# Optimization experiments

Hardware: AMD Instinct MI355X
Metric: run time of the kernel (lower is better)

Reference implementation:

```python
import jax, jax.numpy as jnp
import numpy as np

B, S, D = 8, 1024, 1024
H = 16
HD = D // H
FFN = 4096
BN = 64  # adapter bottleneck
ADAPTER_SCALE = 0.1
EPS = 1e-5


def _ln(x, g, b):
    m = jnp.mean(x, axis=-1, keepdims=True)
    v = jnp.mean(jnp.square(x - m), axis=-1, keepdims=True)
    return (x - m) * jax.lax.rsqrt(v + EPS) * g + b


def setup_inputs() -> dict:
    key = jax.random.key(0)
    ks = jax.random.split(key, 16)
    sd = 0.02
    # weights stored [in, out] (math identical to torch's x @ W.T with W [out,in])
    return {
        "x": jax.random.normal(ks[0], (B, S, D), jnp.float32),
        "ln1_g": jnp.ones((D,), jnp.float32),
        "ln1_b": jnp.zeros((D,), jnp.float32),
        "wq": jax.random.normal(ks[1], (D, D), jnp.float32) * sd,
        "wk": jax.random.normal(ks[2], (D, D), jnp.float32) * sd,
        "wv": jax.random.normal(ks[3], (D, D), jnp.float32) * sd,
        "wo": jax.random.normal(ks[4], (D, D), jnp.float32) * sd,
        "bo": jnp.zeros((D,), jnp.float32),
        "ln2_g": jnp.ones((D,), jnp.float32),
        "ln2_b": jnp.zeros((D,), jnp.float32),
        "w1": jax.random.normal(ks[5], (D, FFN), jnp.float32) * sd,
        "b1": jnp.zeros((FFN,), jnp.float32),
        "w2": jax.random.normal(ks[6], (FFN, D), jnp.float32) * sd,
        "b2": jnp.zeros((D,), jnp.float32),
        "aln_g": jnp.ones((D,), jnp.float32),
        "aln_b": jnp.zeros((D,), jnp.float32),
        "wd": jax.random.normal(ks[7], (D, BN), jnp.float32) * sd,
        "bd": jnp.zeros((BN,), jnp.float32),
        "wu": jax.random.normal(ks[8], (BN, D), jnp.float32) * sd,
        "bu": jnp.zeros((D,), jnp.float32),
    }


def reference(x, ln1_g, ln1_b, wq, wk, wv, wo, bo, ln2_g, ln2_b,
              w1, b1, w2, b2, aln_g, aln_b, wd, bd, wu, bu):
    b, s, d = x.shape
    scale = HD ** -0.5

    # --- attention branch ---
    h = _ln(x, ln1_g, ln1_b)
    q = (h @ wq).reshape(b, s, H, HD)
    k = (h @ wk).reshape(b, s, H, HD)
    v = (h @ wv).reshape(b, s, H, HD)
    scores = jnp.einsum('bqhd,bkhd->bhqk', q, k) * scale  # [B,H,S,S]
    probs = jax.nn.softmax(scores, axis=-1)
    attn = jnp.einsum('bhqk,bkhd->bqhd', probs, v).reshape(b, s, d)
    x = x + (attn @ wo + bo)

    # --- parallel adapter (LN-in, down-relu-up, scaled, no residual) ---
    a = _ln(x, aln_g, aln_b)
    adapt_x = (jax.nn.relu(a @ wd + bd) @ wu + bu) * ADAPTER_SCALE

    # --- MLP branch ---
    residual = x
    h2 = _ln(x, ln2_g, ln2_b)
    h2 = jax.nn.gelu(h2 @ w1 + b1, approximate=False)
    h2 = h2 @ w2 + b2
    h2 = h2 + adapt_x
    return residual + h2
```

## Files before the change

### kernel.cpp

```cpp
#include <hip/hip_runtime.h>
#include <hip/hip_bf16.h>
#include <cstdint>
#include <cstddef>

#define DI __device__ __forceinline__

typedef __attribute__((ext_vector_type(8))) short v8s;
typedef __attribute__((ext_vector_type(4))) float v4f;

DI void gload_lds16(const unsigned short* g, unsigned short* l) {
  __builtin_amdgcn_global_load_lds(
      (const __attribute__((address_space(1))) unsigned int*)g,
      (__attribute__((address_space(3))) unsigned int*)l, 16, 0, 0);
}

DI float bf2f(unsigned short u) { return __uint_as_float(((unsigned int)u) << 16); }
DI unsigned short f2bf(float f) {
  unsigned int u = __float_as_uint(f);
  u += 0x7FFFu + ((u >> 16) & 1u);
  return (unsigned short)(u >> 16);
}
DI unsigned int pack2(float a, float b) {
  return (unsigned int)f2bf(a) | ((unsigned int)f2bf(b) << 16);
}

__global__ __launch_bounds__(256) void transpose_cvt_k(
    const float* __restrict__ in, unsigned short* __restrict__ out, int R, int C) {
  __shared__ unsigned short t[32][33];
  const int j0 = blockIdx.x * 32, i0 = blockIdx.y * 32;
  const int tx = threadIdx.x & 31, ty = threadIdx.x >> 5;
#pragma unroll
  for (int r = 0; r < 32; r += 8) t[ty + r][tx] = f2bf(in[(size_t)(i0 + ty + r) * C + j0 + tx]);
  __syncthreads();
#pragma unroll
  for (int r = 0; r < 32; r += 8) out[(size_t)(j0 + ty + r) * R + i0 + tx] = t[tx][ty + r];
}

__global__ __launch_bounds__(256) void vtrans_k(
    const unsigned short* __restrict__ v, unsigned short* __restrict__ vt, int ld) {
  __shared__ unsigned short t[32][33];
  const int bh = blockIdx.z, b = bh >> 4, h = bh & 15;
  const int s0 = blockIdx.x * 32, d0 = blockIdx.y * 32;
  const int tx = threadIdx.x & 31, ty = threadIdx.x >> 5;
  const unsigned short* src = v + (size_t)(b * 1024 + s0) * ld + h * 64 + d0;
#pragma unroll
  for (int r = 0; r < 32; r += 8) t[ty + r][tx] = src[(size_t)(ty + r) * ld + tx];
  __syncthreads();
  unsigned short* dst = vt + ((size_t)bh * 64 + d0) * 1024 + s0;
#pragma unroll
  for (int r = 0; r < 32; r += 8) dst[(size_t)(ty + r) * 1024 + tx] = t[tx][ty + r];
}

__global__ __launch_bounds__(256) void ln_k(
    const float* __restrict__ x, const float* __restrict__ g,
    const float* __restrict__ b, unsigned short* __restrict__ out) {
  const int row = blockIdx.x;
  const float4 v = ((const float4*)(x + (size_t)row * 1024))[threadIdx.x];
  float s = v.x + v.y + v.z + v.w;
  float ss = v.x * v.x + v.y * v.y + v.z * v.z + v.w * v.w;
#pragma unroll
  for (int o = 1; o < 64; o <<= 1) { s += __shfl_xor(s, o); ss += __shfl_xor(ss, o); }
  __shared__ float red[8];
  const int wid = threadIdx.x >> 6, lane = threadIdx.x & 63;
  if (!lane) { red[wid] = s; red[4 + wid] = ss; }
  __syncthreads();
  s = red[0] + red[1] + red[2] + red[3];
  ss = red[4] + red[5] + red[6] + red[7];
  const float mean = s * (1.f / 1024.f);
  const float var = ss * (1.f / 1024.f) - mean * mean;
  const float rs = rsqrtf(var + 1e-5f);
  const float4 gv = ((const float4*)g)[threadIdx.x];
  const float4 bv = ((const float4*)b)[threadIdx.x];
  ushort4 ov;
  ov.x = f2bf((v.x - mean) * rs * gv.x + bv.x);
  ov.y = f2bf((v.y - mean) * rs * gv.y + bv.y);
  ov.z = f2bf((v.z - mean) * rs * gv.z + bv.z);
  ov.w = f2bf((v.w - mean) * rs * gv.w + bv.w);
  ((ushort4*)(out + (size_t)row * 1024))[threadIdx.x] = ov;
}

enum { EPI_NONE = 0, EPI_BIAS_RES = 1, EPI_GELU = 2, EPI_RELU = 3, EPI_SCALE_BIAS = 4, EPI_FINAL = 5 };

template <int BM, int BN, int EPI, typename CT>
__global__ __launch_bounds__(512, 2) void gemm8_k(
    const unsigned short* __restrict__ A, const unsigned short* __restrict__ Bt,
    CT* __restrict__ C, const float* __restrict__ bias,
    const float* __restrict__ res, const float* __restrict__ extra,
    int M, int N, int K, int gm, int gn) {
  constexpr int MF = BM / 32, NF = BN / 64, MPP = MF / 4;
  constexpr int LA = BM / 64, LB = BN / 64, LT = LA + LB;
  constexpr int BUFE = (BM + BN) * 64;
  __shared__ unsigned short lds[BUFE * 2];
  const int tid = threadIdx.x;
  const int lane = tid & 63, wid = tid >> 6;
  const int wm = wid >> 2, wn = wid & 3;
  const int l15 = lane & 15, l4 = lane >> 4;
  const int nwg = gm * gn;
  const int bid = blockIdx.x;
  const int swz = (bid % 8) * (nwg / 8) + bid / 8;
  const int row0 = (swz / gn) * BM, col0 = (swz % gn) * BN;
  const int NT = K >> 6;

  const int srow = tid >> 3, sgr = tid & 7;
  auto stA = [&](int kt, int b, int a) {
    const unsigned short* s = A + (size_t)(row0 + a * 64 + srow) * K + kt * 64 + ((sgr ^ (srow & 7)) << 3);
    gload_lds16(s, lds + b * BUFE + a * 4096 + tid * 8);
  };
  auto stB = [&](int kt, int b, int a) {
    const unsigned short* s = Bt + (size_t)(col0 + a * 64 + srow) * K + kt * 64 + ((sgr ^ (srow & 7)) << 3);
    gload_lds16(s, lds + b * BUFE + BM * 64 + a * 4096 + tid * 8);
  };

#pragma unroll
  for (int e = 0; e < LA; ++e) stA(0, 0, e);
#pragma unroll
  for (int e = 0; e < LB; ++e) stB(0, 0, e);
#pragma unroll
  for (int e = 0; e < LB; ++e) stB(1, 1, e);
  asm volatile("s_waitcnt vmcnt(%0)" ::"n"(LB) : "memory");
  __builtin_amdgcn_s_barrier();

  v4f acc[MF][NF] = {};
  v8s bfr[NF][2];
  for (int t = 0; t < NT; ++t) {
    const int buf = t & 1;
    const unsigned short* La = lds + buf * BUFE;
    const unsigned short* Lb = lds + buf * BUFE + BM * 64;
#pragma unroll
    for (int p = 0; p < 4; ++p) {
      if (p == 0) {
#pragma unroll
        for (int nf = 0; nf < NF; ++nf) {
          const int r = wn * (BN / 4) + nf * 16 + l15;
#pragma unroll
          for (int kk = 0; kk < 2; ++kk)
            bfr[nf][kk] = *(const v8s*)(Lb + r * 64 + ((kk * 32 + l4 * 8) ^ ((r & 7) << 3)));
        }
      }
      v8s af[MPP][2];
#pragma unroll
      for (int mm = 0; mm < MPP; ++mm) {
        const int r = wm * (BM / 2) + (p * MPP + mm) * 16 + l15;
#pragma unroll
        for (int kk = 0; kk < 2; ++kk)
          af[mm][kk] = *(const v8s*)(La + r * 64 + ((kk * 32 + l4 * 8) ^ ((r & 7) << 3)));
      }
#pragma unroll
      for (int e = p * LT / 4; e < (p + 1) * LT / 4; ++e) {
        if (e < LA) { if (t + 1 < NT) stA(t + 1, buf ^ 1, e); }
        else        { if (t + 2 < NT) stB(t + 2, buf, e - LA); }
      }
      __builtin_amdgcn_s_barrier();
      asm volatile("s_waitcnt lgkmcnt(0)" ::: "memory");
      __builtin_amdgcn_s_setprio(1);
#pragma unroll
      for (int mm = 0; mm < MPP; ++mm)
#pragma unroll
        for (int nf = 0; nf < NF; ++nf)
#pragma unroll
          for (int kk = 0; kk < 2; ++kk)
            acc[p * MPP + mm][nf] = __builtin_amdgcn_mfma_f32_16x16x32_bf16(
                af[mm][kk], bfr[nf][kk], acc[p * MPP + mm][nf], 0, 0, 0);
      __builtin_amdgcn_s_setprio(0);
      if (p == 3 && t + 1 < NT) {
        if (t + 2 < NT) asm volatile("s_waitcnt vmcnt(%0)" ::"n"(LB) : "memory");
        else            asm volatile("s_waitcnt vmcnt(0)" ::: "memory");
      }
      __builtin_amdgcn_s_barrier();
    }
  }

#pragma unroll
  for (int mf = 0; mf < MF; ++mf) {
#pragma unroll
    for (int nf = 0; nf < NF; ++nf) {
      const int col = col0 + wn * (BN / 4) + nf * 16 + l15;
      float bv = 0.f;
      if (EPI != EPI_NONE) bv = bias[col];
#pragma unroll
      for (int j = 0; j < 4; ++j) {
        const int row = row0 + wm * (BM / 2) + mf * 16 + l4 * 4 + j;
        const size_t idx = (size_t)row * N + col;
        float v = acc[mf][nf][j];
        if (EPI == EPI_BIAS_RES) v += bv + res[idx];
        else if (EPI == EPI_GELU) { v += bv; v = 0.5f * v * (1.f + erff(v * 0.70710678118f)); }
        else if (EPI == EPI_RELU) { v += bv; v = fmaxf(v, 0.f); }
        else if (EPI == EPI_SCALE_BIAS) { v = (v + bv) * 0.1f; }
        else if (EPI == EPI_FINAL) { v += bv + res[idx] + extra[idx]; }
        if constexpr (sizeof(CT) == 2) C[idx] = f2bf(v); else C[idx] = v;
      }
    }
  }
}

template <int BN, int EPI, typename CT>
__global__ __launch_bounds__(256) void gemm_k(
    const unsigned short* __restrict__ A, const unsigned short* __restrict__ Bt,
    CT* __restrict__ C, const float* __restrict__ bias,
    const float* __restrict__ res, const float* __restrict__ extra,
    int M, int N, int K) {
  constexpr int BM = 128, BK = 32;
  constexpr int WN = (BN == 128) ? 2 : 1;
  constexpr int MR = (BN == 128) ? 4 : 2;
  constexpr int NR = 4;
  __shared__ unsigned short sA[BM * BK];
  __shared__ unsigned short sB[BN * BK];
  const int tid = threadIdx.x;
  const int lane = tid & 63, wid = tid >> 6;
  const int wm = wid / WN, wn = wid % WN;
  const int l15 = lane & 15, l4 = lane >> 4;
  const int row0 = blockIdx.x * BM, col0 = blockIdx.y * BN;
  v4f acc[MR][NR] = {};
  const int rowA = wm * MR * 16;
  const int rowB = wn * NR * 16;
  for (int k0 = 0; k0 < K; k0 += BK) {
#pragma unroll
    for (int r = 0; r < (BM * BK) / (256 * 8); ++r) {
      int e = (r * 256 + tid) * 8;
      gload_lds16(A + (size_t)(row0 + (e >> 5)) * K + k0 + (e & 31), ((unsigned short*)sA) + e);
    }
#pragma unroll
    for (int r = 0; r < (BN * BK) / (256 * 8); ++r) {
      int e = (r * 256 + tid) * 8;
      gload_lds16(Bt + (size_t)(col0 + (e >> 5)) * K + k0 + (e & 31), ((unsigned short*)sB) + e);
    }
    __syncthreads();
    v8s af[MR], bfr2[NR];
#pragma unroll
    for (int m = 0; m < MR; ++m) af[m] = *(const v8s*)(sA + (rowA + m * 16 + l15) * BK + l4 * 8);
#pragma unroll
    for (int n = 0; n < NR; ++n) bfr2[n] = *(const v8s*)(sB + (rowB + n * 16 + l15) * BK + l4 * 8);
#pragma unroll
    for (int m = 0; m < MR; ++m)
#pragma unroll
      for (int n = 0; n < NR; ++n)
        acc[m][n] = __builtin_amdgcn_mfma_f32_16x16x32_bf16(af[m], bfr2[n], acc[m][n], 0, 0, 0);
    __syncthreads();
  }
#pragma unroll
  for (int m = 0; m < MR; ++m) {
#pragma unroll
    for (int n = 0; n < NR; ++n) {
      const int col = col0 + rowB + n * 16 + l15;
      float bv = 0.f;
      if (EPI != EPI_NONE) bv = bias[col];
#pragma unroll
      for (int j = 0; j < 4; ++j) {
        const int row = row0 + rowA + m * 16 + l4 * 4 + j;
        const size_t idx = (size_t)row * N + col;
        float v = acc[m][n][j];
        if (EPI == EPI_BIAS_RES) v += bv + res[idx];
        else if (EPI == EPI_GELU) { v += bv; v = 0.5f * v * (1.f + erff(v * 0.70710678118f)); }
        else if (EPI == EPI_RELU) { v += bv; v = fmaxf(v, 0.f); }
        else if (EPI == EPI_SCALE_BIAS) { v = (v + bv) * 0.1f; }
        else if (EPI == EPI_FINAL) { v += bv + res[idx] + extra[idx]; }
        if constexpr (sizeof(CT) == 2) C[idx] = f2bf(v); else C[idx] = v;
      }
    }
  }
}

__global__ __launch_bounds__(256) void attn_k(
    const unsigned short* __restrict__ Q, const unsigned short* __restrict__ Kc,
    const unsigned short* __restrict__ VT, unsigned short* __restrict__ O, int ldqk) {
  const int bh = blockIdx.y, b = bh >> 4, h = bh & 15;
  const int q0 = blockIdx.x * 64;
  const int tid = threadIdx.x, lane = tid & 63, wid = tid >> 6;
  const int l15 = lane & 15, l4 = lane >> 4;
  __shared__ unsigned short sQ[64 * 64];
  __shared__ unsigned short sK[32 * 64];
  __shared__ unsigned short sV[64 * 32];
  const unsigned short* Qb = Q + (size_t)(b * 1024 + q0) * ldqk + h * 64;
  const unsigned short* Kb = Kc + (size_t)(b * 1024) * ldqk + h * 64;
  const unsigned short* Vb = VT + (size_t)bh * 64 * 1024;
#pragma unroll
  for (int r = 0; r < 2; ++r) {
    int e = (r * 256 + tid) * 8, qr = e >> 6, gs = ((e >> 3) & 7) ^ (qr & 7);
    gload_lds16(Qb + (size_t)qr * ldqk + gs * 8, ((unsigned short*)sQ) + e);
  }
  float m_run = -3e38f, l_run = 0.f;
  v4f oacc[4] = {};
  const int qrow = wid * 16 + l15;
  for (int k0 = 0; k0 < 1024; k0 += 32) {
    { int e = tid * 8, kr = e >> 6, gs = ((e >> 3) & 7) ^ (kr & 7);
      gload_lds16(Kb + (size_t)(k0 + kr) * ldqk + gs * 8, ((unsigned short*)sK) + e); }
    { int e = tid * 8, dr = e >> 5, gs = ((e >> 3) & 3) ^ (dr & 3) ^ ((dr >> 2) & 3);
      gload_lds16(Vb + (size_t)dr * 1024 + k0 + gs * 8, ((unsigned short*)sV) + e); }
    __syncthreads();
    v4f sc0 = {}, sc1 = {};
#pragma unroll
    for (int dh = 0; dh < 2; ++dh) {
      const int ga0 = (l4 + 4 * dh) ^ (l15 & 7);
      v8s a0 = *(const v8s*)(sK + l15 * 64 + ga0 * 8);
      const int kr1 = 16 + l15;
      const int ga1 = (l4 + 4 * dh) ^ (kr1 & 7);
      v8s a1 = *(const v8s*)(sK + kr1 * 64 + ga1 * 8);
      const int gb = (l4 + 4 * dh) ^ (qrow & 7);
      v8s bq = *(const v8s*)(sQ + qrow * 64 + gb * 8);
      sc0 = __builtin_amdgcn_mfma_f32_16x16x32_bf16(a0, bq, sc0, 0, 0, 0);
      sc1 = __builtin_amdgcn_mfma_f32_16x16x32_bf16(a1, bq, sc1, 0, 0, 0);
    }
    float s8[8];
    float smax = -3e38f;
#pragma unroll
    for (int j = 0; j < 4; ++j) { s8[j] = sc0[j] * 0.125f; s8[4 + j] = sc1[j] * 0.125f; }
#pragma unroll
    for (int i = 0; i < 8; ++i) smax = fmaxf(smax, s8[i]);
    smax = fmaxf(smax, __shfl_xor(smax, 16));
    smax = fmaxf(smax, __shfl_xor(smax, 32));
    const float m_new = fmaxf(m_run, smax);
    const float fac = __expf(m_run - m_new);
    float tsum = 0.f;
#pragma unroll
    for (int i = 0; i < 8; ++i) { s8[i] = __expf(s8[i] - m_new); tsum += s8[i]; }
    tsum += __shfl_xor(tsum, 16);
    tsum += __shfl_xor(tsum, 32);
    l_run = l_run * fac + tsum;
    m_run = m_new;
#pragma unroll
    for (int nb = 0; nb < 4; ++nb) {
      oacc[nb][0] *= fac; oacc[nb][1] *= fac; oacc[nb][2] *= fac; oacc[nb][3] *= fac;
    }
    const unsigned int w0 = pack2(s8[0], s8[1]), w1 = pack2(s8[2], s8[3]);
    const unsigned int w2 = pack2(s8[4], s8[5]), w3 = pack2(s8[6], s8[7]);
    const int cse = l4 >> 1;
    const int src0 = l15 + 32 * (l4 & 1);
    const int src1 = src0 + 16;
    const unsigned int t00 = __shfl((int)w0, src0), t20 = __shfl((int)w2, src0);
    const unsigned int t10 = __shfl((int)w1, src0), t30 = __shfl((int)w3, src0);
    const unsigned int t01 = __shfl((int)w0, src1), t21 = __shfl((int)w2, src1);
    const unsigned int t11 = __shfl((int)w1, src1), t31 = __shfl((int)w3, src1);
    union { unsigned int u[4]; v8s v; } pb;
    pb.u[0] = cse ? t20 : t00; pb.u[1] = cse ? t30 : t10;
    pb.u[2] = cse ? t21 : t01; pb.u[3] = cse ? t31 : t11;
#pragma unroll
    for (int nb = 0; nb < 4; ++nb) {
      const int drow = nb * 16 + l15;
      const int gv = l4 ^ (drow & 3) ^ ((drow >> 2) & 3);
      v8s vf = *(const v8s*)(sV + drow * 32 + gv * 8);
      oacc[nb] = __builtin_amdgcn_mfma_f32_16x16x32_bf16(vf, pb.v, oacc[nb], 0, 0, 0);
    }
    __syncthreads();
  }
  const float inv = 1.f / l_run;
  unsigned short* Or = O + (size_t)(b * 1024 + q0 + wid * 16 + l15) * 1024 + h * 64;
#pragma unroll
  for (int nb = 0; nb < 4; ++nb) {
    ushort4 st;
    st.x = f2bf(oacc[nb][0] * inv); st.y = f2bf(oacc[nb][1] * inv);
    st.z = f2bf(oacc[nb][2] * inv); st.w = f2bf(oacc[nb][3] * inv);
    *(ushort4*)(Or + nb * 16 + l4 * 4) = st;
  }
}

extern "C" void kernel_launch(void* const* d_in, const int* in_sizes, int n_in,
                              void* d_out, int out_size, void* d_ws, size_t ws_size,
                              hipStream_t stream) {
  (void)in_sizes; (void)n_in; (void)out_size;
  const float* x    = (const float*)d_in[0];
  const float* ln1g = (const float*)d_in[1];
  const float* ln1b = (const float*)d_in[2];
  const float* wq   = (const float*)d_in[3];
  const float* wk   = (const float*)d_in[4];
  const float* wv   = (const float*)d_in[5];
  const float* wo   = (const float*)d_in[6];
  const float* bo   = (const float*)d_in[7];
  const float* ln2g = (const float*)d_in[8];
  const float* ln2b = (const float*)d_in[9];
  const float* w1   = (const float*)d_in[10];
  const float* b1   = (const float*)d_in[11];
  const float* w2   = (const float*)d_in[12];
  const float* b2   = (const float*)d_in[13];
  const float* alng = (const float*)d_in[14];
  const float* alnb = (const float*)d_in[15];
  const float* wd   = (const float*)d_in[16];
  const float* bd   = (const float*)d_in[17];
  const float* wu   = (const float*)d_in[18];
  const float* bu   = (const float*)d_in[19];
  float* out = (float*)d_out;

  char* W = (char*)d_ws;
  size_t off = 0;
  auto allocB = [&](size_t bytes) { void* p = W + off; off += (bytes + 255) & ~(size_t)255; return p; };
  const size_t T = 8192;
  unsigned short* wqkvt = (unsigned short*)allocB((size_t)3072 * 1024 * 2);
  unsigned short* wot   = (unsigned short*)allocB((size_t)1024 * 1024 * 2);
  unsigned short* w1t   = (unsigned short*)allocB((size_t)4096 * 1024 * 2);
  unsigned short* w2t   = (unsigned short*)allocB((size_t)4096 * 1024 * 2);
  unsigned short* wdt   = (unsigned short*)allocB(64 * 1024 * 2);
  unsigned short* wut   = (unsigned short*)allocB(64 * 1024 * 2);
  unsigned short* H     = (unsigned short*)allocB(T * 1024 * 2);
  unsigned short* QKV   = (unsigned short*)allocB(T * 3072 * 2);
  unsigned short* VT    = (unsigned short*)allocB(T * 1024 * 2);
  float* X2             = (float*)allocB(T * 1024 * 4);
  unsigned short* MID   = (unsigned short*)allocB(T * 4096 * 2);
  unsigned short* AO  = MID;
  unsigned short* DWN = VT;
  float* ADP          = (float*)QKV;
  if (ws_size < off) return;

  dim3 blk(256);
  transpose_cvt_k<<<dim3(32, 32), blk, 0, stream>>>(wq, wqkvt, 1024, 1024);
  transpose_cvt_k<<<dim3(32, 32), blk, 0, stream>>>(wk, wqkvt + (size_t)1024 * 1024, 1024, 1024);
  transpose_cvt_k<<<dim3(32, 32), blk, 0, stream>>>(wv, wqkvt + (size_t)2048 * 1024, 1024, 1024);
  transpose_cvt_k<<<dim3(32, 32), blk, 0, stream>>>(wo, wot, 1024, 1024);
  transpose_cvt_k<<<dim3(128, 32), blk, 0, stream>>>(w1, w1t, 1024, 4096);
  transpose_cvt_k<<<dim3(32, 128), blk, 0, stream>>>(w2, w2t, 4096, 1024);
  transpose_cvt_k<<<dim3(2, 32), blk, 0, stream>>>(wd, wdt, 1024, 64);
  transpose_cvt_k<<<dim3(32, 2), blk, 0, stream>>>(wu, wut, 64, 1024);

  ln_k<<<8192, blk, 0, stream>>>(x, ln1g, ln1b, H);
  gemm8_k<128, 256, EPI_NONE, unsigned short><<<768, 512, 0, stream>>>(
      H, wqkvt, QKV, nullptr, nullptr, nullptr, 8192, 3072, 1024, 64, 12);
  vtrans_k<<<dim3(32, 2, 128), blk, 0, stream>>>(QKV + 2048, VT, 3072);
  attn_k<<<dim3(16, 128), blk, 0, stream>>>(QKV, QKV + 1024, VT, AO, 3072);
  gemm8_k<128, 256, EPI_BIAS_RES, float><<<256, 512, 0, stream>>>(
      AO, wot, X2, bo, x, nullptr, 8192, 1024, 1024, 64, 4);
  ln_k<<<8192, blk, 0, stream>>>(X2, alng, alnb, H);
  gemm_k<64, EPI_RELU, unsigned short><<<dim3(64, 1), blk, 0, stream>>>(
      H, wdt, DWN, bd, nullptr, nullptr, 8192, 64, 1024);
  gemm_k<128, EPI_SCALE_BIAS, float><<<dim3(64, 8), blk, 0, stream>>>(
      DWN, wut, ADP, bu, nullptr, nullptr, 8192, 1024, 64);
  ln_k<<<8192, blk, 0, stream>>>(X2, ln2g, ln2b, H);
  gemm8_k<256, 256, EPI_GELU, unsigned short><<<512, 512, 0, stream>>>(
      H, w1t, MID, b1, nullptr, nullptr, 8192, 4096, 1024, 32, 16);
  gemm8_k<128, 256, EPI_FINAL, float><<<256, 512, 0, stream>>>(
      MID, w2t, out, b2, X2, ADP, 8192, 1024, 4096, 64, 4);
}
```

Before: 613.4 us.

## Rewrite attention with 32x32 MFMA, register Q, double-buffered K/V; fuse dual LayerNorm

```diff
diff --git a/kernel.cpp b/kernel.cpp
--- a/kernel.cpp
+++ b/kernel.cpp
@@ -7,6 +7,7 @@
 
 typedef __attribute__((ext_vector_type(8))) short v8s;
 typedef __attribute__((ext_vector_type(4))) float v4f;
+typedef __attribute__((ext_vector_type(16))) float v16f;
 
 DI void gload_lds16(const unsigned short* g, unsigned short* l) {
   __builtin_amdgcn_global_load_lds(
@@ -19,9 +20,6 @@
   unsigned int u = __float_as_uint(f);
   u += 0x7FFFu + ((u >> 16) & 1u);
   return (unsigned short)(u >> 16);
-}
-DI unsigned int pack2(float a, float b) {
-  return (unsigned int)f2bf(a) | ((unsigned int)f2bf(b) << 16);
 }
 
 __global__ __launch_bounds__(256) void transpose_cvt_k(
@@ -79,6 +77,40 @@
   ((ushort4*)(out + (size_t)row * 1024))[threadIdx.x] = ov;
 }
 
+__global__ __launch_bounds__(256) void ln_dual_k(
+    const float* __restrict__ x, const float* __restrict__ g1, const float* __restrict__ b1,
+    const float* __restrict__ g2, const float* __restrict__ b2,
+    unsigned short* __restrict__ o1, unsigned short* __restrict__ o2) {
+  const int row = blockIdx.x;
+  const float4 v = ((const float4*)(x + (size_t)row * 1024))[threadIdx.x];
+  float s = v.x + v.y + v.z + v.w;
+  float ss = v.x * v.x + v.y * v.y + v.z * v.z + v.w * v.w;
+#pragma unroll
+  for (int o = 1; o < 64; o <<= 1) { s += __shfl_xor(s, o); ss += __shfl_xor(ss, o); }
+  __shared__ float red[8];
+  const int wid = threadIdx.x >> 6, lane = threadIdx.x & 63;
+  if (!lane) { red[wid] = s; red[4 + wid] = ss; }
+  __syncthreads();
+  s = red[0] + red[1] + red[2] + red[3];
+  ss = red[4] + red[5] + red[6] + red[7];
+  const float mean = s * (1.f / 1024.f);
+  const float var = ss * (1.f / 1024.f) - mean * mean;
+  const float rs = rsqrtf(var + 1e-5f);
+  const float n0 = (v.x - mean) * rs, n1 = (v.y - mean) * rs, n2 = (v.z - mean) * rs, n3 = (v.w - mean) * rs;
+  {
+    const float4 gv = ((const float4*)g1)[threadIdx.x];
+    const float4 bv = ((const float4*)b1)[threadIdx.x];
+    ushort4 ov{f2bf(n0 * gv.x + bv.x), f2bf(n1 * gv.y + bv.y), f2bf(n2 * gv.z + bv.z), f2bf(n3 * gv.w + bv.w)};
+    ((ushort4*)(o1 + (size_t)row * 1024))[threadIdx.x] = ov;
+  }
+  {
+    const float4 gv = ((const float4*)g2)[threadIdx.x];
+    const float4 bv = ((const float4*)b2)[threadIdx.x];
+    ushort4 ov{f2bf(n0 * gv.x + bv.x), f2bf(n1 * gv.y + bv.y), f2bf(n2 * gv.z + bv.z), f2bf(n3 * gv.w + bv.w)};
+    ((ushort4*)(o2 + (size_t)row * 1024))[threadIdx.x] = ov;
+  }
+}
+
 enum { EPI_NONE = 0, EPI_BIAS_RES = 1, EPI_GELU = 2, EPI_RELU = 3, EPI_SCALE_BIAS = 4, EPI_FINAL = 5 };
 
 template <int BM, int BN, int EPI, typename CT>
@@ -87,7 +119,9 @@
     CT* __restrict__ C, const float* __restrict__ bias,
     const float* __restrict__ res, const float* __restrict__ extra,
     int M, int N, int K, int gm, int gn) {
-  constexpr int MF = BM / 32, NF = BN / 64, MPP = MF / 4;
+  constexpr int MF = BM / 32, NF = BN / 64;
+  constexpr int PH = (MF * NF) / 8 < 1 ? 1 : (MF * NF) / 8;
+  constexpr int MPP = MF / PH;
   constexpr int LA = BM / 64, LB = BN / 64, LT = LA + LB;
   constexpr int BUFE = (BM + BN) * 64;
   __shared__ unsigned short lds[BUFE * 2];
@@ -115,9 +149,13 @@
   for (int e = 0; e < LA; ++e) stA(0, 0, e);
 #pragma unroll
   for (int e = 0; e < LB; ++e) stB(0, 0, e);
-#pragma unroll
-  for (int e = 0; e < LB; ++e) stB(1, 1, e);
-  asm volatile("s_waitcnt vmcnt(%0)" ::"n"(LB) : "memory");
+  if (NT > 1) {
+#pragma unroll
+    for (int e = 0; e < LB; ++e) stB(1, 1, e);
+    asm volatile("s_waitcnt vmcnt(%0)" ::"n"(LB) : "memory");
+  } else {
+    asm volatile("s_waitcnt vmcnt(0)" ::: "memory");
+  }
   __builtin_amdgcn_s_barrier();
 
   v4f acc[MF][NF] = {};
@@ -127,7 +165,7 @@
     const unsigned short* La = lds + buf * BUFE;
     const unsigned short* Lb = lds + buf * BUFE + BM * 64;
 #pragma unroll
-    for (int p = 0; p < 4; ++p) {
+    for (int p = 0; p < PH; ++p) {
       if (p == 0) {
 #pragma unroll
         for (int nf = 0; nf < NF; ++nf) {
@@ -146,7 +184,7 @@
           af[mm][kk] = *(const v8s*)(La + r * 64 + ((kk * 32 + l4 * 8) ^ ((r & 7) << 3)));
       }
 #pragma unroll
-      for (int e = p * LT / 4; e < (p + 1) * LT / 4; ++e) {
+      for (int e = p * LT / PH; e < (p + 1) * LT / PH; ++e) {
         if (e < LA) { if (t + 1 < NT) stA(t + 1, buf ^ 1, e); }
         else        { if (t + 2 < NT) stB(t + 2, buf, e - LA); }
       }
@@ -162,7 +200,7 @@
             acc[p * MPP + mm][nf] = __builtin_amdgcn_mfma_f32_16x16x32_bf16(
                 af[mm][kk], bfr[nf][kk], acc[p * MPP + mm][nf], 0, 0, 0);
       __builtin_amdgcn_s_setprio(0);
-      if (p == 3 && t + 1 < NT) {
+      if (p == PH - 1 && t + 1 < NT) {
         if (t + 2 < NT) asm volatile("s_waitcnt vmcnt(%0)" ::"n"(LB) : "memory");
         else            asm volatile("s_waitcnt vmcnt(0)" ::: "memory");
       }
@@ -261,95 +299,116 @@
 }
 
 __global__ __launch_bounds__(256) void attn_k(
-    const unsigned short* __restrict__ Q, const unsigned short* __restrict__ Kc,
-    const unsigned short* __restrict__ VT, unsigned short* __restrict__ O, int ldqk) {
-  const int bh = blockIdx.y, b = bh >> 4, h = bh & 15;
-  const int q0 = blockIdx.x * 64;
-  const int tid = threadIdx.x, lane = tid & 63, wid = tid >> 6;
-  const int l15 = lane & 15, l4 = lane >> 4;
-  __shared__ unsigned short sQ[64 * 64];
-  __shared__ unsigned short sK[32 * 64];
-  __shared__ unsigned short sV[64 * 32];
-  const unsigned short* Qb = Q + (size_t)(b * 1024 + q0) * ldqk + h * 64;
-  const unsigned short* Kb = Kc + (size_t)(b * 1024) * ldqk + h * 64;
-  const unsigned short* Vb = VT + (size_t)bh * 64 * 1024;
-#pragma unroll
-  for (int r = 0; r < 2; ++r) {
-    int e = (r * 256 + tid) * 8, qr = e >> 6, gs = ((e >> 3) & 7) ^ (qr & 7);
-    gload_lds16(Qb + (size_t)qr * ldqk + gs * 8, ((unsigned short*)sQ) + e);
-  }
+    const unsigned short* __restrict__ QKV, const unsigned short* __restrict__ VT,
+    unsigned short* __restrict__ O) {
+  const int bid = blockIdx.x;
+  const int swz = (bid & 7) * 128 + (bid >> 3);
+  const int bh = swz >> 3, qb = swz & 7;
+  const int b = bh >> 4, h = bh & 15;
+  const int tid = threadIdx.x, lane = tid & 63, w = tid >> 6;
+  const int l31 = lane & 31, hi = lane >> 5;
+  __shared__ unsigned short sK[2][64 * 64];
+  __shared__ unsigned short sV[2][64 * 64];
+  const int q0 = qb * 128;
+  const unsigned short* Qrow = QKV + (size_t)(b * 1024 + q0 + w * 32 + l31) * 3072 + h * 64;
+  v8s qf[4];
+#pragma unroll
+  for (int kcd = 0; kcd < 4; ++kcd) qf[kcd] = *(const v8s*)(Qrow + kcd * 16 + hi * 8);
+
+  const unsigned short* Kbase = QKV + 1024 + (size_t)(b * 1024) * 3072 + h * 64;
+  const unsigned short* Vbase = VT + (size_t)bh * 64 * 1024;
+  const int sr = tid >> 3, sg = tid & 7;
+  auto stage = [&](int t, int bsel) {
+    const int k0 = t * 64;
+#pragma unroll
+    for (int ps = 0; ps < 2; ++ps) {
+      const int r = ps * 32 + sr;
+      gload_lds16(Kbase + (size_t)(k0 + r) * 3072 + ((sg ^ (r & 7)) << 3), &sK[bsel][r * 64 + sg * 8]);
+    }
+#pragma unroll
+    for (int ps = 0; ps < 2; ++ps) {
+      const int r = ps * 32 + sr;
+      gload_lds16(Vbase + (size_t)r * 1024 + k0 + ((sg ^ (r & 7)) << 3), &sV[bsel][r * 64 + sg * 8]);
+    }
+  };
+  stage(0, 0);
+  asm volatile("s_waitcnt vmcnt(0)" ::: "memory");
+  __syncthreads();
+
+  const float SC = 0.125f * 1.44269504f;
   float m_run = -3e38f, l_run = 0.f;
-  v4f oacc[4] = {};
-  const int qrow = wid * 16 + l15;
-  for (int k0 = 0; k0 < 1024; k0 += 32) {
-    { int e = tid * 8, kr = e >> 6, gs = ((e >> 3) & 7) ^ (kr & 7);
-      gload_lds16(Kb + (size_t)(k0 + kr) * ldqk + gs * 8, ((unsigned short*)sK) + e); }
-    { int e = tid * 8, dr = e >> 5, gs = ((e >> 3) & 3) ^ (dr & 3) ^ ((dr >> 2) & 3);
-      gload_lds16(Vb + (size_t)dr * 1024 + k0 + gs * 8, ((unsigned short*)sV) + e); }
-    __syncthreads();
-    v4f sc0 = {}, sc1 = {};
-#pragma unroll
-    for (int dh = 0; dh < 2; ++dh) {
-      const int ga0 = (l4 + 4 * dh) ^ (l15 & 7);
-      v8s a0 = *(const v8s*)(sK + l15 * 64 + ga0 * 8);
-      const int kr1 = 16 + l15;
-      const int ga1 = (l4 + 4 * dh) ^ (kr1 & 7);
-      v8s a1 = *(const v8s*)(sK + kr1 * 64 + ga1 * 8);
-      const int gb = (l4 + 4 * dh) ^ (qrow & 7);
-      v8s bq = *(const v8s*)(sQ + qrow * 64 + gb * 8);
-      sc0 = __builtin_amdgcn_mfma_f32_16x16x32_bf16(a0, bq, sc0, 0, 0, 0);
-      sc1 = __builtin_amdgcn_mfma_f32_16x16x32_bf16(a1, bq, sc1, 0, 0, 0);
-    }
-    float s8[8];
-    float smax = -3e38f;
-#pragma unroll
-    for (int j = 0; j < 4; ++j) { s8[j] = sc0[j] * 0.125f; s8[4 + j] = sc1[j] * 0.125f; }
-#pragma unroll
-    for (int i = 0; i < 8; ++i) smax = fmaxf(smax, s8[i]);
-    smax = fmaxf(smax, __shfl_xor(smax, 16));
-    smax = fmaxf(smax, __shfl_xor(smax, 32));
-    const float m_new = fmaxf(m_run, smax);
-    const float fac = __expf(m_run - m_new);
-    float tsum = 0.f;
-#pragma unroll
-    for (int i = 0; i < 8; ++i) { s8[i] = __expf(s8[i] - m_new); tsum += s8[i]; }
-    tsum += __shfl_xor(tsum, 16);
-    tsum += __shfl_xor(tsum, 32);
-    l_run = l_run * fac + tsum;
+  v16f oacc0 = {}, oacc1 = {};
+
+  for (int t = 0; t < 16; ++t) {
+    const int cur = t & 1;
+    if (t + 1 < 16) stage(t + 1, cur ^ 1);
+    v16f s0 = {}, s1 = {};
+#pragma unroll
+    for (int kcd = 0; kcd < 4; ++kcd) {
+      const int c = kcd * 2 + hi;
+      v8s a0 = *(const v8s*)(&sK[cur][l31 * 64 + ((c ^ (l31 & 7)) << 3)]);
+      v8s a1 = *(const v8s*)(&sK[cur][(32 + l31) * 64 + ((c ^ (l31 & 7)) << 3)]);
+      s0 = __builtin_amdgcn_mfma_f32_32x32x16_bf16(a0, qf[kcd], s0, 0, 0, 0);
+      s1 = __builtin_amdgcn_mfma_f32_32x32x16_bf16(a1, qf[kcd], s1, 0, 0, 0);
+    }
+    float p0[16], p1[16];
+#pragma unroll
+    for (int i = 0; i < 16; ++i) { p0[i] = s0[i] * SC; p1[i] = s1[i] * SC; }
+    float mx = fmaxf(p0[0], p1[0]);
+#pragma unroll
+    for (int i = 1; i < 16; ++i) mx = fmaxf(mx, fmaxf(p0[i], p1[i]));
+    mx = fmaxf(mx, __shfl_xor(mx, 32));
+    const float m_new = fmaxf(m_run, mx);
+    const float fac = exp2f(m_run - m_new);
+    float ts = 0.f;
+#pragma unroll
+    for (int i = 0; i < 16; ++i) {
+      p0[i] = exp2f(p0[i] - m_new);
+      p1[i] = exp2f(p1[i] - m_new);
+      ts += p0[i] + p1[i];
+    }
+    ts += __shfl_xor(ts, 32);
+    l_run = l_run * fac + ts;
     m_run = m_new;
 #pragma unroll
-    for (int nb = 0; nb < 4; ++nb) {
-      oacc[nb][0] *= fac; oacc[nb][1] *= fac; oacc[nb][2] *= fac; oacc[nb][3] *= fac;
-    }
-    const unsigned int w0 = pack2(s8[0], s8[1]), w1 = pack2(s8[2], s8[3]);
-    const unsigned int w2 = pack2(s8[4], s8[5]), w3 = pack2(s8[6], s8[7]);
-    const int cse = l4 >> 1;
-    const int src0 = l15 + 32 * (l4 & 1);
-    const int src1 = src0 + 16;
-    const unsigned int t00 = __shfl((int)w0, src0), t20 = __shfl((int)w2, src0);
-    const unsigned int t10 = __shfl((int)w1, src0), t30 = __shfl((int)w3, src0);
-    const unsigned int t01 = __shfl((int)w0, src1), t21 = __shfl((int)w2, src1);
-    const unsigned int t11 = __shfl((int)w1, src1), t31 = __shfl((int)w3, src1);
-    union { unsigned int u[4]; v8s v; } pb;
-    pb.u[0] = cse ? t20 : t00; pb.u[1] = cse ? t30 : t10;
-    pb.u[2] = cse ? t21 : t01; pb.u[3] = cse ? t31 : t11;
-#pragma unroll
-    for (int nb = 0; nb < 4; ++nb) {
-      const int drow = nb * 16 + l15;
-      const int gv = l4 ^ (drow & 3) ^ ((drow >> 2) & 3);
-      v8s vf = *(const v8s*)(sV + drow * 32 + gv * 8);
-      oacc[nb] = __builtin_amdgcn_mfma_f32_16x16x32_bf16(vf, pb.v, oacc[nb], 0, 0, 0);
-    }
-    __syncthreads();
+    for (int i = 0; i < 16; ++i) { oacc0[i] *= fac; oacc1[i] *= fac; }
+    auto mkfrag = [&](const float* p, int c) -> v8s {
+      unsigned A0, A1, A2, A3;
+      asm("v_cvt_pk_bf16_f32 %0, %1, %2" : "=v"(A0) : "v"(p[8 * c + 0]), "v"(p[8 * c + 1]));
+      asm("v_cvt_pk_bf16_f32 %0, %1, %2" : "=v"(A1) : "v"(p[8 * c + 2]), "v"(p[8 * c + 3]));
+      asm("v_cvt_pk_bf16_f32 %0, %1, %2" : "=v"(A2) : "v"(p[8 * c + 4]), "v"(p[8 * c + 5]));
+      asm("v_cvt_pk_bf16_f32 %0, %1, %2" : "=v"(A3) : "v"(p[8 * c + 6]), "v"(p[8 * c + 7]));
+      asm("v_permlane32_swap_b32 %0, %1" : "+v"(A2), "+v"(A0));
+      asm("v_permlane32_swap_b32 %0, %1" : "+v"(A3), "+v"(A1));
+      union { unsigned u[4]; v8s v; } r;
+      r.u[0] = A0; r.u[1] = A1; r.u[2] = A2; r.u[3] = A3;
+      return r.v;
+    };
+    v8s pB0 = mkfrag(p0, 0), pB1 = mkfrag(p0, 1), pB2 = mkfrag(p1, 0), pB3 = mkfrag(p1, 1);
+#pragma unroll
+    for (int kc = 0; kc < 4; ++kc) {
+      const v8s pb = (kc == 0) ? pB0 : (kc == 1) ? pB1 : (kc == 2) ? pB2 : pB3;
+      const int c = kc * 2 + hi;
+      v8s vf0 = *(const v8s*)(&sV[cur][l31 * 64 + ((c ^ (l31 & 7)) << 3)]);
+      v8s vf1 = *(const v8s*)(&sV[cur][(32 + l31) * 64 + ((c ^ (l31 & 7)) << 3)]);
+      oacc0 = __builtin_amdgcn_mfma_f32_32x32x16_bf16(vf0, pb, oacc0, 0, 0, 0);
+      oacc1 = __builtin_amdgcn_mfma_f32_32x32x16_bf16(vf1, pb, oacc1, 0, 0, 0);
+    }
+    if (t + 1 < 16) {
+      asm volatile("s_waitcnt vmcnt(0)" ::: "memory");
+      __syncthreads();
+    }
   }
   const float inv = 1.f / l_run;
-  unsigned short* Or = O + (size_t)(b * 1024 + q0 + wid * 16 + l15) * 1024 + h * 64;
-#pragma unroll
-  for (int nb = 0; nb < 4; ++nb) {
-    ushort4 st;
-    st.x = f2bf(oacc[nb][0] * inv); st.y = f2bf(oacc[nb][1] * inv);
-    st.z = f2bf(oacc[nb][2] * inv); st.w = f2bf(oacc[nb][3] * inv);
-    *(ushort4*)(Or + nb * 16 + l4 * 4) = st;
+  unsigned short* Orow = O + (size_t)(b * 1024 + q0 + w * 32 + l31) * 1024 + h * 64;
+#pragma unroll
+  for (int g = 0; g < 4; ++g) {
+    ushort4 st0{f2bf(oacc0[4 * g + 0] * inv), f2bf(oacc0[4 * g + 1] * inv),
+                f2bf(oacc0[4 * g + 2] * inv), f2bf(oacc0[4 * g + 3] * inv)};
+    ushort4 st1{f2bf(oacc1[4 * g + 0] * inv), f2bf(oacc1[4 * g + 1] * inv),
+                f2bf(oacc1[4 * g + 2] * inv), f2bf(oacc1[4 * g + 3] * inv)};
+    *(ushort4*)(Orow + g * 8 + hi * 4) = st0;
+    *(ushort4*)(Orow + 32 + g * 8 + hi * 4) = st1;
   }
 }
 
@@ -390,6 +449,7 @@
   unsigned short* wdt   = (unsigned short*)allocB(64 * 1024 * 2);
   unsigned short* wut   = (unsigned short*)allocB(64 * 1024 * 2);
   unsigned short* H     = (unsigned short*)allocB(T * 1024 * 2);
+  unsigned short* H2    = (unsigned short*)allocB(T * 1024 * 2);
   unsigned short* QKV   = (unsigned short*)allocB(T * 3072 * 2);
   unsigned short* VT    = (unsigned short*)allocB(T * 1024 * 2);
   float* X2             = (float*)allocB(T * 1024 * 4);
@@ -413,17 +473,16 @@
   gemm8_k<128, 256, EPI_NONE, unsigned short><<<768, 512, 0, stream>>>(
       H, wqkvt, QKV, nullptr, nullptr, nullptr, 8192, 3072, 1024, 64, 12);
   vtrans_k<<<dim3(32, 2, 128), blk, 0, stream>>>(QKV + 2048, VT, 3072);
-  attn_k<<<dim3(16, 128), blk, 0, stream>>>(QKV, QKV + 1024, VT, AO, 3072);
+  attn_k<<<1024, blk, 0, stream>>>(QKV, VT, AO);
   gemm8_k<128, 256, EPI_BIAS_RES, float><<<256, 512, 0, stream>>>(
       AO, wot, X2, bo, x, nullptr, 8192, 1024, 1024, 64, 4);
-  ln_k<<<8192, blk, 0, stream>>>(X2, alng, alnb, H);
+  ln_dual_k<<<8192, blk, 0, stream>>>(X2, alng, alnb, ln2g, ln2b, H, H2);
   gemm_k<64, EPI_RELU, unsigned short><<<dim3(64, 1), blk, 0, stream>>>(
       H, wdt, DWN, bd, nullptr, nullptr, 8192, 64, 1024);
   gemm_k<128, EPI_SCALE_BIAS, float><<<dim3(64, 8), blk, 0, stream>>>(
       DWN, wut, ADP, bu, nullptr, nullptr, 8192, 1024, 64);
-  ln_k<<<8192, blk, 0, stream>>>(X2, ln2g, ln2b, H);
   gemm8_k<256, 256, EPI_GELU, unsigned short><<<512, 512, 0, stream>>>(
-      H, w1t, MID, b1, nullptr, nullptr, 8192, 4096, 1024, 32, 16);
+      H2, w1t, MID, b1, nullptr, nullptr, 8192, 4096, 1024, 32, 16);
   gemm8_k<128, 256, EPI_FINAL, float><<<256, 512, 0, stream>>>(
       MID, w2t, out, b2, X2, ADP, 8192, 1024, 4096, 64, 4);
 }
```

Measured after the change: 570.4 us. 7.0% less time.
